# Kernel tuning notes

Measured on AMD Instinct MI355X. Metric: run time of the kernel, lower is better.

The kernel has to match this reference:

```python
import jax, jax.numpy as jnp
from jax import lax
import numpy as np

B, N, C, HEADS = 8, 4096, 512, 16
HD = C // HEADS


def rope2d(x, h, w, base=10000.0):
    # x: [b, h, w, c]; 2D axial RoPE as in the torch `rope` helper
    c = x.shape[-1]
    k_max = c // 4  # feature_dim // (2 * len(channel_dims))
    theta = 1.0 / (base ** (jnp.arange(k_max, dtype=jnp.float32) / k_max))  # [k_max]
    ii = jnp.arange(h, dtype=jnp.float32)[:, None, None]  # row index
    jj = jnp.arange(w, dtype=jnp.float32)[None, :, None]  # col index
    ang = jnp.concatenate([
        jnp.broadcast_to(ii * theta, (h, w, k_max)),
        jnp.broadcast_to(jj * theta, (h, w, k_max)),
    ], axis=-1)  # [h, w, c//2]
    cos, sin = jnp.cos(ang), jnp.sin(ang)
    xp = x.reshape(x.shape[0], h, w, c // 2, 2)
    xr, xi = xp[..., 0], xp[..., 1]
    out = jnp.stack([xr * cos - xi * sin, xi * cos + xr * sin], axis=-1)
    return out.reshape(x.shape)


def setup_inputs() -> dict:
    key = jax.random.key(0)
    k1, k2, k3, k4, k5 = jax.random.split(key, 5)
    x = jax.random.normal(k1, (B, N, C), dtype=jnp.float32)
    Wqk = jax.random.normal(k2, (C, 2 * C), dtype=jnp.float32) * 0.02
    bqk = jax.random.normal(k3, (2 * C,), dtype=jnp.float32) * 0.02
    lepe_w = jax.random.normal(k4, (C, 1, 3, 3), dtype=jnp.float32) * 0.05  # depthwise OIHW
    lepe_b = jax.random.normal(k5, (C,), dtype=jnp.float32) * 0.02
    return {"x": x, "h": 64, "w": 64, "Wqk": Wqk, "bqk": bqk, "lepe_w": lepe_w, "lepe_b": lepe_b}


def reference(x, h, w, Wqk, bqk, lepe_w, lepe_b):
    b, n, c = x.shape
    hd = c // HEADS
    qk = x @ Wqk + bqk                       # [b, n, 2c]
    q = jax.nn.elu(qk[..., :c]) + 1.0        # ELU+1 feature map
    k = jax.nn.elu(qk[..., c:]) + 1.0
    v = x
    q_rope = rope2d(q.reshape(b, h, w, c), h, w).reshape(b, n, HEADS, hd)
    k_rope = rope2d(k.reshape(b, h, w, c), h, w).reshape(b, n, HEADS, hd)
    qh = q.reshape(b, n, HEADS, hd)
    kh = k.reshape(b, n, HEADS, hd)
    vh = v.reshape(b, n, HEADS, hd)
    k_mean = kh.mean(axis=1)                 # [b, HEADS, hd]
    z = 1.0 / (jnp.einsum('bnhd,bhd->bnh', qh, k_mean) + 1e-6)  # [b, n, HEADS]
    inv_n = 1.0 / jnp.float32(n)
    kv = jnp.einsum('bnhd,bnhe->bhde', k_rope, vh) * inv_n       # [b, HEADS, hd, hd]
    attn = jnp.einsum('bnhd,bhde->bnhe', q_rope, kv) * z[..., None]
    out = attn.reshape(b, n, c)
    # depthwise 3x3 LePE on v (== x) as NCHW image
    v_img = x.reshape(b, h, w, c).transpose(0, 3, 1, 2)
    lepe = lax.conv_general_dilated(v_img, lepe_w, (1, 1), 'SAME',
                                    feature_group_count=c,
                                    dimension_numbers=('NCHW', 'OIHW', 'NCHW'))
    lepe = lepe + lepe_b[None, :, None, None]
    out = out + lepe.transpose(0, 2, 3, 1).reshape(b, n, c)
    return out
```

## Files before the change

kernel.cpp:

```cpp
#include <hip/hip_runtime.h>
#include <stdint.h>

static constexpr int BATCH = 8;
static constexpr int NTOK  = 4096;
static constexpr int CDIM  = 512;
static constexpr int NCOL  = 1024;
static constexpr int MROWS = BATCH * NTOK;
static constexpr int KDIM  = 512;

static constexpr size_t OFF_KSUM = 0;
static constexpr size_t OFF_KV   = 16384;
static constexpr size_t OFF_XB   = 540672;
static constexpr size_t OFF_WT   = OFF_XB + 33554432;
static constexpr size_t OFF_QP   = OFF_WT + 1048576;
static constexpr size_t OFF_KR   = OFF_QP + 33554432;
static constexpr size_t OFF_TRIG = OFF_KR + 33554432;
static constexpr size_t OFF_WT9  = OFF_TRIG + 65536;
static constexpr size_t WS_NEED  = OFF_WT9 + 18432;

static constexpr int KV_CHUNKS = 64;
static constexpr int KV_OUT    = BATCH * 16 * 32 * 32;

typedef __attribute__((ext_vector_type(8))) short bf16x8;
typedef __attribute__((ext_vector_type(4))) float f32x4;
typedef __attribute__((ext_vector_type(8))) unsigned short u16x8;

__device__ __forceinline__ float bf2f(unsigned short u) {
  union { unsigned int i; float f; } v; v.i = ((unsigned int)u) << 16; return v.f;
}
__device__ __forceinline__ unsigned short f2bf(float f) {
  union { float f; unsigned int i; } v; v.f = f;
  unsigned int b = v.i + 0x7FFFu + ((v.i >> 16) & 1u);
  return (unsigned short)(b >> 16);
}
__device__ __forceinline__ void gload16(const void* g, void* l) {
  __builtin_amdgcn_global_load_lds(
      (const __attribute__((address_space(1))) unsigned int*)g,
      (__attribute__((address_space(3))) unsigned int*)l,
      16, 0, 0);
}
__device__ __forceinline__ float elu1(float v) {
  return v > 0.f ? v + 1.f : __expf(v);
}

__global__ void prep_kernel(const float* __restrict__ x, const float* __restrict__ Wqk,
                            const float* __restrict__ lepe_w,
                            float* __restrict__ wsf, unsigned short* __restrict__ xb,
                            unsigned short* __restrict__ wT, float2* __restrict__ trig,
                            float* __restrict__ wt9) {
  const int ZN = (int)(OFF_XB / 4);
  const int XN = MROWS * CDIM / 8;
  const int WN = (KDIM * NCOL) / 8;
  const int TN = 64 * 128;
  const int W9 = 9 * 512;
  const int total = ZN + XN + WN + TN + W9;
  for (int i = blockIdx.x * blockDim.x + threadIdx.x; i < total;
       i += gridDim.x * blockDim.x) {
    if (i < ZN) {
      wsf[i] = 0.f;
    } else if (i < ZN + XN) {
      const int j = i - ZN;
      const float4* xp = (const float4*)x + (size_t)j * 2;
      const float4 a = xp[0], b4 = xp[1];
      u16x8 o;
      o[0] = f2bf(a.x);  o[1] = f2bf(a.y);  o[2] = f2bf(a.z);  o[3] = f2bf(a.w);
      o[4] = f2bf(b4.x); o[5] = f2bf(b4.y); o[6] = f2bf(b4.z); o[7] = f2bf(b4.w);
      *((u16x8*)xb + j) = o;
    } else if (i < ZN + XN + WN) {
      const int j = i - ZN - XN;
      const int nc8 = j & 127;
      const int k   = j >> 7;
      const float4* wp = (const float4*)(Wqk + (size_t)k * NCOL + nc8 * 8);
      const float4 a = wp[0], b4 = wp[1];
      const float vals[8] = {a.x, a.y, a.z, a.w, b4.x, b4.y, b4.z, b4.w};
      const int nc0 = nc8 * 8;
#pragma unroll
      for (int t = 0; t < 8; ++t) wT[(size_t)(nc0 + t) * KDIM + k] = f2bf(vals[t]);
    } else if (i < ZN + XN + WN + TN) {
      const int j = i - ZN - XN - WN;
      const int tt = j & 127;
      const int pos = j >> 7;
      const float theta = __expf(-(float)tt * 0.07195578415f);
      const float ang = (float)pos * theta;
      float s, c;
      sincosf(ang, &s, &c);
      trig[pos * 128 + tt] = make_float2(c, s);
    } else {
      const int j = i - ZN - XN - WN - TN;
      const int tap = j >> 9;
      const int c   = j & 511;
      wt9[tap * 512 + c] = lepe_w[c * 9 + tap];
    }
  }
}

__global__ __launch_bounds__(256)
void gemm_kernel(const unsigned short* __restrict__ xb, const unsigned short* __restrict__ wT,
                 const float* __restrict__ bqk, const float2* __restrict__ trig,
                 unsigned short* __restrict__ qp, unsigned short* __restrict__ kr,
                 float* __restrict__ ksum) {
  __shared__ __align__(16) unsigned short S[3][2][128 * 32];
  float* Cst = (float*)&S[0][0][0];
  const int tid = threadIdx.x;
  const int w = tid >> 6;
  const int l = tid & 63;
  const int m0 = blockIdx.x * 128;
  const int nidx = blockIdx.y;
  const int n0 = nidx * 128;
  const int wr = w >> 1, wc = w & 1;

  f32x4 acc[4][4];
#pragma unroll
  for (int i = 0; i < 4; ++i)
#pragma unroll
    for (int j = 0; j < 4; ++j) acc[i][j] = (f32x4){0.f, 0.f, 0.f, 0.f};

  const int c0 = w * 2, c1 = w * 2 + 1;
  const int lr = l >> 2;
  const int lk = (l & 3) * 8;
  const int la = l & 15, lg = l >> 4;
  const int lb = lg * 8;

#define STAGE(kt, bb) do {                                                        \
    const int kc_ = (kt) * 32 + lk;                                               \
    gload16(xb + (size_t)(m0 + c0 * 16 + lr) * KDIM + kc_, &S[bb][0][c0 * 512]);  \
    gload16(xb + (size_t)(m0 + c1 * 16 + lr) * KDIM + kc_, &S[bb][0][c1 * 512]);  \
    gload16(wT + (size_t)(n0 + c0 * 16 + lr) * KDIM + kc_, &S[bb][1][c0 * 512]);  \
    gload16(wT + (size_t)(n0 + c1 * 16 + lr) * KDIM + kc_, &S[bb][1][c1 * 512]);  \
  } while (0)

  STAGE(0, 0);
  STAGE(1, 1);
  asm volatile("s_waitcnt vmcnt(4)" ::: "memory");
  __builtin_amdgcn_s_barrier();
  __builtin_amdgcn_sched_barrier(0);

#pragma unroll
  for (int kt = 0; kt < KDIM / 32; ++kt) {
    const int cur = kt % 3;
    if (kt + 2 < KDIM / 32) STAGE(kt + 2, (kt + 2) % 3);
    bf16x8 af[4], bfr[4];
#pragma unroll
    for (int mi = 0; mi < 4; ++mi)
      af[mi] = *(const bf16x8*)&S[cur][0][(wr * 64 + mi * 16 + la) * 32 + lb];
#pragma unroll
    for (int ni = 0; ni < 4; ++ni)
      bfr[ni] = *(const bf16x8*)&S[cur][1][(wc * 64 + ni * 16 + la) * 32 + lb];
#pragma unroll
    for (int mi = 0; mi < 4; ++mi)
#pragma unroll
      for (int ni = 0; ni < 4; ++ni)
        acc[mi][ni] = __builtin_amdgcn_mfma_f32_16x16x32_bf16(af[mi], bfr[ni], acc[mi][ni], 0, 0, 0);
    if (kt < KDIM / 32 - 1) {
      if (kt + 2 < KDIM / 32) {
        asm volatile("s_waitcnt vmcnt(4)" ::: "memory");
      } else {
        asm volatile("s_waitcnt vmcnt(0)" ::: "memory");
      }
      __builtin_amdgcn_s_barrier();
      __builtin_amdgcn_sched_barrier(0);
    }
  }
#undef STAGE

  const bool isq = (nidx < 4);
  const int bidx = m0 >> 12;
  float colsum[4] = {0.f, 0.f, 0.f, 0.f};
#pragma unroll
  for (int ni = 0; ni < 4; ++ni) {
    const int colg = n0 + wc * 64 + ni * 16 + la;
    const float bias = bqk[colg];
#pragma unroll
    for (int mi = 0; mi < 4; ++mi) {
#pragma unroll
      for (int r = 0; r < 4; ++r) {
        const float v = elu1(acc[mi][ni][r] + bias);
        acc[mi][ni][r] = v;
        if (!isq) colsum[ni] += v;
      }
    }
  }
  if (!isq) {
#pragma unroll
    for (int ni = 0; ni < 4; ++ni) {
      float s = colsum[ni];
      s += __shfl_xor(s, 16);
      s += __shfl_xor(s, 32);
      if (lg == 0) {
        const int ck = n0 - 512 + wc * 64 + ni * 16 + la;
        atomicAdd(&ksum[bidx * CDIM + ck], s);
      }
    }
  }

  for (int cc = 0; cc < 4; ++cc) {
    __syncthreads();
    if (wr == (cc >> 1)) {
      const int mi0 = (cc & 1) * 2;
#pragma unroll
      for (int mil = 0; mil < 2; ++mil) {
#pragma unroll
        for (int ni = 0; ni < 4; ++ni) {
#pragma unroll
          for (int r = 0; r < 4; ++r) {
            Cst[(mil * 16 + lg * 4 + r) * 132 + wc * 64 + ni * 16 + la] = acc[mi0 + mil][ni][r];
          }
        }
      }
    }
    __syncthreads();
#pragma unroll
    for (int it = 0; it < 2; ++it) {
      const int idx = it * 256 + tid;
      const int rowloc = idx >> 4;
      const int seg = idx & 15;
      const int grow = m0 + cc * 32 + rowloc;
      const int lcol = seg * 8;
      float v[8];
      *(float2*)&v[0] = *(const float2*)&Cst[rowloc * 132 + lcol + 0];
      *(float2*)&v[2] = *(const float2*)&Cst[rowloc * 132 + lcol + 2];
      *(float2*)&v[4] = *(const float2*)&Cst[rowloc * 132 + lcol + 4];
      *(float2*)&v[6] = *(const float2*)&Cst[rowloc * 132 + lcol + 6];
      if (isq) {
        u16x8 o;
#pragma unroll
        for (int j = 0; j < 8; ++j) o[j] = f2bf(v[j]);
        *(u16x8*)(qp + (size_t)grow * CDIM + n0 + lcol) = o;
      } else {
        const int ck0 = n0 - 512 + lcol;
        const int n = grow & (NTOK - 1);
        const int p0 = ck0 >> 1;
        const int pos = (p0 >= 128) ? (n & 63) : (n >> 6);
        const float4 t01 = *(const float4*)&trig[pos * 128 + p0];
        const float4 t23 = *(const float4*)&trig[pos * 128 + p0 + 2];
        u16x8 o;
        o[0] = f2bf(v[0] * t01.x - v[1] * t01.y);
        o[1] = f2bf(v[1] * t01.x + v[0] * t01.y);
        o[2] = f2bf(v[2] * t01.z - v[3] * t01.w);
        o[3] = f2bf(v[3] * t01.z + v[2] * t01.w);
        o[4] = f2bf(v[4] * t23.x - v[5] * t23.y);
        o[5] = f2bf(v[5] * t23.x + v[4] * t23.y);
        o[6] = f2bf(v[6] * t23.z - v[7] * t23.w);
        o[7] = f2bf(v[7] * t23.z + v[6] * t23.w);
        *(u16x8*)(kr + (size_t)grow * CDIM + ck0) = o;
      }
    }
  }
}

__global__ __launch_bounds__(512)
void kvpart_kernel(const unsigned short* __restrict__ kr, const unsigned short* __restrict__ xb,
                   float* __restrict__ part) {
  const int bid = blockIdx.x;
  const int b = bid >> 6, ch = bid & 63;
  const int t = threadIdx.x;
  const int h = t >> 5;
  const int sub = t & 31;
  const int d0 = (sub >> 2) * 4, e0 = (sub & 3) * 8;

  float acc[4][8];
#pragma unroll
  for (int i = 0; i < 4; ++i)
#pragma unroll
    for (int j = 0; j < 8; ++j) acc[i][j] = 0.f;

  const size_t rowbase = (size_t)(b * NTOK + ch * 64) * CDIM + h * 32;
  ushort4 k4 = *(const ushort4*)(kr + rowbase + d0);
  u16x8 v8 = *(const u16x8*)(xb + rowbase + e0);
#pragma unroll 2
  for (int r = 0; r < 64; ++r) {
    ushort4 kn = k4;
    u16x8 vn = v8;
    if (r < 63) {
      const size_t offn = rowbase + (size_t)(r + 1) * CDIM;
      kn = *(const ushort4*)(kr + offn + d0);
      vn = *(const u16x8*)(xb + offn + e0);
    }
    const float kf0 = bf2f(k4.x), kf1 = bf2f(k4.y), kf2 = bf2f(k4.z), kf3 = bf2f(k4.w);
    float vf[8];
#pragma unroll
    for (int j = 0; j < 8; ++j) vf[j] = bf2f(v8[j]);
#pragma unroll
    for (int j = 0; j < 8; ++j) {
      acc[0][j] += kf0 * vf[j];
      acc[1][j] += kf1 * vf[j];
      acc[2][j] += kf2 * vf[j];
      acc[3][j] += kf3 * vf[j];
    }
    k4 = kn;
    v8 = vn;
  }

  float* p = part + ((size_t)ch * BATCH * 16 + b * 16 + h) * 1024;
#pragma unroll
  for (int i = 0; i < 4; ++i) {
    *(float4*)&p[(d0 + i) * 32 + e0 + 0] = *(float4*)&acc[i][0];
    *(float4*)&p[(d0 + i) * 32 + e0 + 4] = *(float4*)&acc[i][4];
  }
}

__global__ __launch_bounds__(256)
void kvred_kernel(const float* __restrict__ part, float* __restrict__ kv) {
  const int o = blockIdx.x * 256 + threadIdx.x;
  float s0 = 0.f, s1 = 0.f, s2 = 0.f, s3 = 0.f;
#pragma unroll
  for (int ch = 0; ch < KV_CHUNKS; ch += 4) {
    s0 += part[(size_t)(ch + 0) * KV_OUT + o];
    s1 += part[(size_t)(ch + 1) * KV_OUT + o];
    s2 += part[(size_t)(ch + 2) * KV_OUT + o];
    s3 += part[(size_t)(ch + 3) * KV_OUT + o];
  }
  kv[o] = (s0 + s1 + s2 + s3) * (1.0f / (float)NTOK);
}

__global__ __launch_bounds__(256)
void out4_kernel(const unsigned short* __restrict__ qp, const float* __restrict__ ksum,
                 const float* __restrict__ kv, const float2* __restrict__ trig,
                 const unsigned short* __restrict__ xb, const float* __restrict__ wt9,
                 const float* __restrict__ lepe_b, float* __restrict__ out) {
  __shared__ __align__(16) float kvs[32 * 32];
  __shared__ __align__(16) float qrs[32 * 40];
  const int y = blockIdx.x;
  const int h = blockIdx.y >> 1, half = blockIdx.y & 1;
  const int b = blockIdx.z;
  const int t = threadIdx.x;
  const int e8 = t & 7, tok = t >> 3;
  const int c4 = e8 * 4;

  ((float4*)kvs)[t] = ((const float4*)(kv + (size_t)(b * 16 + h) * 1024))[t];

  const float4 ks4 = *(const float4*)(ksum + b * CDIM + h * 32 + c4);
  const float4 lb4 = *(const float4*)(lepe_b + h * 32 + c4);
  float4 w4[9];
#pragma unroll
  for (int tap = 0; tap < 9; ++tap)
    w4[tap] = *(const float4*)(wt9 + tap * CDIM + h * 32 + c4);
  const int pbase = (h * 16 + e8 * 2) & 127;
  __syncthreads();

  const float inv_n = 1.0f / (float)NTOK;
  const int col = half * 32 + tok;
  const int n = y * 64 + col;
  const size_t rowoff = ((size_t)(b * NTOK + n)) * CDIM + h * 32;

  const ushort4 q4u = *(const ushort4*)(qp + rowoff + c4);
  const float q0 = bf2f(q4u.x), q1 = bf2f(q4u.y), q2 = bf2f(q4u.z), q3 = bf2f(q4u.w);
  float zs = q0 * ks4.x + q1 * ks4.y + q2 * ks4.z + q3 * ks4.w;
  zs += __shfl_xor(zs, 1);
  zs += __shfl_xor(zs, 2);
  zs += __shfl_xor(zs, 4);
  const float z = 1.0f / (zs * inv_n + 1e-6f);
  const int pos = (h >= 8) ? col : y;
  const float4 cs01 = *(const float4*)&trig[pos * 128 + pbase];
  float4 qr;
  qr.x = q0 * cs01.x - q1 * cs01.y;
  qr.y = q1 * cs01.x + q0 * cs01.y;
  qr.z = q2 * cs01.z - q3 * cs01.w;
  qr.w = q3 * cs01.z + q2 * cs01.w;
  *(float4*)&qrs[tok * 40 + c4] = qr;
  float4 acc = lb4;
#pragma unroll
  for (int dy = 0; dy < 3; ++dy) {
    const int iy = y + dy - 1;
    if (iy < 0 || iy > 63) continue;
#pragma unroll
    for (int dx = 0; dx < 3; ++dx) {
      const int ix = col + dx - 1;
      if (ix < 0 || ix > 63) continue;
      const ushort4 xv = *(const ushort4*)(xb + ((size_t)(b * NTOK) + iy * 64 + ix) * CDIM + h * 32 + c4);
      const float4 wv = w4[dy * 3 + dx];
      acc.x += bf2f(xv.x) * wv.x; acc.y += bf2f(xv.y) * wv.y;
      acc.z += bf2f(xv.z) * wv.z; acc.w += bf2f(xv.w) * wv.w;
    }
  }
  float4 attn = {0.f, 0.f, 0.f, 0.f};
#pragma unroll
  for (int dg = 0; dg < 8; ++dg) {
    const float4 qv = *(const float4*)&qrs[tok * 40 + dg * 4];
#pragma unroll
    for (int j = 0; j < 4; ++j) {
      const float qs = (j == 0) ? qv.x : (j == 1) ? qv.y : (j == 2) ? qv.z : qv.w;
      const float4 kvr = *(const float4*)&kvs[(dg * 4 + j) * 32 + c4];
      attn.x += qs * kvr.x; attn.y += qs * kvr.y;
      attn.z += qs * kvr.z; attn.w += qs * kvr.w;
    }
  }
  float4 res;
  res.x = attn.x * z + acc.x;
  res.y = attn.y * z + acc.y;
  res.z = attn.z * z + acc.z;
  res.w = attn.w * z + acc.w;
  *(float4*)(out + rowoff + c4) = res;
}

extern "C" void kernel_launch(void* const* d_in, const int* in_sizes, int n_in,
                              void* d_out, int out_size, void* d_ws, size_t ws_size,
                              hipStream_t stream) {
  const float* x      = (const float*)d_in[0];
  const float* Wqk    = (const float*)d_in[3];
  const float* bqk    = (const float*)d_in[4];
  const float* lepe_w = (const float*)d_in[5];
  const float* lepe_b = (const float*)d_in[6];
  float* out = (float*)d_out;

  if (ws_size < WS_NEED) return;

  char* ws = (char*)d_ws;
  float* ksum            = (float*)(ws + OFF_KSUM);
  float* kv              = (float*)(ws + OFF_KV);
  unsigned short* xb     = (unsigned short*)(ws + OFF_XB);
  unsigned short* wT     = (unsigned short*)(ws + OFF_WT);
  unsigned short* qp     = (unsigned short*)(ws + OFF_QP);
  unsigned short* kr     = (unsigned short*)(ws + OFF_KR);
  float2* trig           = (float2*)(ws + OFF_TRIG);
  float* wt9             = (float*)(ws + OFF_WT9);
  float* part            = (float*)d_out;

  hipLaunchKernelGGL(prep_kernel, dim3(2048), dim3(256), 0, stream,
                     x, Wqk, lepe_w, (float*)ws, xb, wT, trig, wt9);
  hipLaunchKernelGGL(gemm_kernel, dim3(MROWS / 128, NCOL / 128), dim3(256), 0, stream,
                     xb, wT, bqk, trig, qp, kr, ksum);
  hipLaunchKernelGGL(kvpart_kernel, dim3(BATCH * KV_CHUNKS), dim3(512), 0, stream,
                     kr, xb, part);
  hipLaunchKernelGGL(kvred_kernel, dim3(KV_OUT / 256), dim3(256), 0, stream,
                     part, kv);
  hipLaunchKernelGGL(out4_kernel, dim3(64, 32, 8), dim3(256), 0, stream,
                     qp, ksum, kv, trig, xb, wt9, lepe_b, out);
}
```

Before: 172.7 us.

## Enlarge QK GEMM tile to 256x256 with 8 waves and interleaved staging

The QK projection GEMM now uses 512-thread blocks that each compute a 256x256 output tile, so every staged A and B slice is reused across more MFMAs. Each k-step is split into two MFMA halves, with the global-to-LDS loads for A and then B interleaved between them. The MFMA phases run under raised wave priority (s_setprio), and the grid is reordered so that blocks sharing the same row tile are adjacent, which should help L2 reuse of x. The trig lookup index for the RoPE epilogue is also masked to 128 entries, which changes which table entries are read. The costs are more accumulator registers per thread, larger LDS use, and fewer blocks in the grid.

```diff
diff --git a/kernel.cpp b/kernel.cpp
--- a/kernel.cpp
+++ b/kernel.cpp
@@ -94,116 +94,128 @@
   }
 }
 
-__global__ __launch_bounds__(256)
+__global__ __launch_bounds__(512)
 void gemm_kernel(const unsigned short* __restrict__ xb, const unsigned short* __restrict__ wT,
                  const float* __restrict__ bqk, const float2* __restrict__ trig,
                  unsigned short* __restrict__ qp, unsigned short* __restrict__ kr,
                  float* __restrict__ ksum) {
-  __shared__ __align__(16) unsigned short S[3][2][128 * 32];
+  __shared__ __align__(16) unsigned short S[3][2][8192];
   float* Cst = (float*)&S[0][0][0];
   const int tid = threadIdx.x;
-  const int w = tid >> 6;
+  const int wid = tid >> 6;
   const int l = tid & 63;
-  const int m0 = blockIdx.x * 128;
-  const int nidx = blockIdx.y;
-  const int n0 = nidx * 128;
-  const int wr = w >> 1, wc = w & 1;
-
-  f32x4 acc[4][4];
-#pragma unroll
-  for (int i = 0; i < 4; ++i)
+  const int la = l & 15, lg = l >> 4;
+  const int wm = wid >> 2, wn = wid & 3;
+  const int nt = blockIdx.x;
+  const int m0 = blockIdx.y * 256;
+  const int n0 = nt * 256;
+
+  f32x4 acc[8][4];
+#pragma unroll
+  for (int i = 0; i < 8; ++i)
 #pragma unroll
     for (int j = 0; j < 4; ++j) acc[i][j] = (f32x4){0.f, 0.f, 0.f, 0.f};
 
-  const int c0 = w * 2, c1 = w * 2 + 1;
-  const int lr = l >> 2;
-  const int lk = (l & 3) * 8;
-  const int la = l & 15, lg = l >> 4;
-  const int lb = lg * 8;
-
-#define STAGE(kt, bb) do {                                                        \
-    const int kc_ = (kt) * 32 + lk;                                               \
-    gload16(xb + (size_t)(m0 + c0 * 16 + lr) * KDIM + kc_, &S[bb][0][c0 * 512]);  \
-    gload16(xb + (size_t)(m0 + c1 * 16 + lr) * KDIM + kc_, &S[bb][0][c1 * 512]);  \
-    gload16(wT + (size_t)(n0 + c0 * 16 + lr) * KDIM + kc_, &S[bb][1][c0 * 512]);  \
-    gload16(wT + (size_t)(n0 + c1 * 16 + lr) * KDIM + kc_, &S[bb][1][c1 * 512]);  \
-  } while (0)
-
-  STAGE(0, 0);
-  STAGE(1, 1);
+  const int srow = tid >> 2;
+  const int scol = (tid & 3) * 8;
+
+#define STG_A(kt, bb, rr) gload16(xb + (size_t)(m0 + (rr) * 128 + srow) * KDIM + (kt) * 32 + scol, \
+                                  &S[bb][0][(rr) * 4096 + tid * 8])
+#define STG_B(kt, bb, rr) gload16(wT + (size_t)(n0 + (rr) * 128 + srow) * KDIM + (kt) * 32 + scol, \
+                                  &S[bb][1][(rr) * 4096 + tid * 8])
+
+  STG_A(0, 0, 0); STG_A(0, 0, 1); STG_B(0, 0, 0); STG_B(0, 0, 1);
+  STG_A(1, 1, 0); STG_A(1, 1, 1); STG_B(1, 1, 0); STG_B(1, 1, 1);
   asm volatile("s_waitcnt vmcnt(4)" ::: "memory");
   __builtin_amdgcn_s_barrier();
   __builtin_amdgcn_sched_barrier(0);
 
-#pragma unroll
-  for (int kt = 0; kt < KDIM / 32; ++kt) {
+  for (int kt = 0; kt < 16; ++kt) {
     const int cur = kt % 3;
-    if (kt + 2 < KDIM / 32) STAGE(kt + 2, (kt + 2) % 3);
-    bf16x8 af[4], bfr[4];
-#pragma unroll
-    for (int mi = 0; mi < 4; ++mi)
-      af[mi] = *(const bf16x8*)&S[cur][0][(wr * 64 + mi * 16 + la) * 32 + lb];
-#pragma unroll
-    for (int ni = 0; ni < 4; ++ni)
-      bfr[ni] = *(const bf16x8*)&S[cur][1][(wc * 64 + ni * 16 + la) * 32 + lb];
-#pragma unroll
-    for (int mi = 0; mi < 4; ++mi)
-#pragma unroll
-      for (int ni = 0; ni < 4; ++ni)
-        acc[mi][ni] = __builtin_amdgcn_mfma_f32_16x16x32_bf16(af[mi], bfr[ni], acc[mi][ni], 0, 0, 0);
-    if (kt < KDIM / 32 - 1) {
-      if (kt + 2 < KDIM / 32) {
-        asm volatile("s_waitcnt vmcnt(4)" ::: "memory");
-      } else {
-        asm volatile("s_waitcnt vmcnt(0)" ::: "memory");
-      }
-      __builtin_amdgcn_s_barrier();
-      __builtin_amdgcn_sched_barrier(0);
-    }
-  }
-#undef STAGE
-
-  const bool isq = (nidx < 4);
+    const int nx2 = (kt + 2) % 3;
+    bf16x8 af[4], bf[4];
+#pragma unroll
+    for (int i = 0; i < 4; ++i)
+      af[i] = *(const bf16x8*)&S[cur][0][(wm * 128 + i * 16 + la) * 32 + lg * 8];
+#pragma unroll
+    for (int j = 0; j < 4; ++j)
+      bf[j] = *(const bf16x8*)&S[cur][1][(wn * 64 + j * 16 + la) * 32 + lg * 8];
+    if (kt + 2 < 16) { STG_A(kt + 2, nx2, 0); STG_A(kt + 2, nx2, 1); }
+    __builtin_amdgcn_s_barrier();
+    asm volatile("s_waitcnt lgkmcnt(0)" ::: "memory");
+    __builtin_amdgcn_sched_barrier(0);
+    __builtin_amdgcn_s_setprio(1);
+#pragma unroll
+    for (int i = 0; i < 4; ++i)
+#pragma unroll
+      for (int j = 0; j < 4; ++j)
+        acc[i][j] = __builtin_amdgcn_mfma_f32_16x16x32_bf16(af[i], bf[j], acc[i][j], 0, 0, 0);
+    __builtin_amdgcn_s_setprio(0);
+    __builtin_amdgcn_s_barrier();
+#pragma unroll
+    for (int i = 0; i < 4; ++i)
+      af[i] = *(const bf16x8*)&S[cur][0][(wm * 128 + (4 + i) * 16 + la) * 32 + lg * 8];
+    if (kt + 2 < 16) { STG_B(kt + 2, nx2, 0); STG_B(kt + 2, nx2, 1); }
+    __builtin_amdgcn_s_barrier();
+    asm volatile("s_waitcnt lgkmcnt(0)" ::: "memory");
+    __builtin_amdgcn_sched_barrier(0);
+    __builtin_amdgcn_s_setprio(1);
+#pragma unroll
+    for (int i = 0; i < 4; ++i)
+#pragma unroll
+      for (int j = 0; j < 4; ++j)
+        acc[4 + i][j] = __builtin_amdgcn_mfma_f32_16x16x32_bf16(af[i], bf[j], acc[4 + i][j], 0, 0, 0);
+    __builtin_amdgcn_s_setprio(0);
+    if (kt < 14) {
+      asm volatile("s_waitcnt vmcnt(4)" ::: "memory");
+    } else if (kt == 14) {
+      asm volatile("s_waitcnt vmcnt(0)" ::: "memory");
+    }
+    __builtin_amdgcn_s_barrier();
+    __builtin_amdgcn_sched_barrier(0);
+  }
+#undef STG_A
+#undef STG_B
+
+  const bool isq = (nt < 2);
   const int bidx = m0 >> 12;
   float colsum[4] = {0.f, 0.f, 0.f, 0.f};
 #pragma unroll
-  for (int ni = 0; ni < 4; ++ni) {
-    const int colg = n0 + wc * 64 + ni * 16 + la;
-    const float bias = bqk[colg];
-#pragma unroll
-    for (int mi = 0; mi < 4; ++mi) {
+  for (int j = 0; j < 4; ++j) {
+    const float bias = bqk[n0 + wn * 64 + j * 16 + la];
+#pragma unroll
+    for (int i = 0; i < 8; ++i) {
 #pragma unroll
       for (int r = 0; r < 4; ++r) {
-        const float v = elu1(acc[mi][ni][r] + bias);
-        acc[mi][ni][r] = v;
-        if (!isq) colsum[ni] += v;
+        const float v = elu1(acc[i][j][r] + bias);
+        acc[i][j][r] = v;
+        if (!isq) colsum[j] += v;
       }
     }
   }
   if (!isq) {
 #pragma unroll
-    for (int ni = 0; ni < 4; ++ni) {
-      float s = colsum[ni];
+    for (int j = 0; j < 4; ++j) {
+      float s = colsum[j];
       s += __shfl_xor(s, 16);
       s += __shfl_xor(s, 32);
       if (lg == 0) {
-        const int ck = n0 - 512 + wc * 64 + ni * 16 + la;
-        atomicAdd(&ksum[bidx * CDIM + ck], s);
+        atomicAdd(&ksum[bidx * CDIM + (n0 - 512) + wn * 64 + j * 16 + la], s);
       }
     }
   }
 
-  for (int cc = 0; cc < 4; ++cc) {
+  for (int cc = 0; cc < 8; ++cc) {
     __syncthreads();
-    if (wr == (cc >> 1)) {
-      const int mi0 = (cc & 1) * 2;
+    if (wm == (cc >> 2)) {
+      const int mi0 = (cc & 3) * 2;
 #pragma unroll
       for (int mil = 0; mil < 2; ++mil) {
 #pragma unroll
-        for (int ni = 0; ni < 4; ++ni) {
+        for (int j = 0; j < 4; ++j) {
 #pragma unroll
           for (int r = 0; r < 4; ++r) {
-            Cst[(mil * 16 + lg * 4 + r) * 132 + wc * 64 + ni * 16 + la] = acc[mi0 + mil][ni][r];
+            Cst[(mil * 16 + lg * 4 + r) * 260 + wn * 64 + j * 16 + la] = acc[mi0 + mil][j][r];
           }
         }
       }
@@ -211,28 +223,28 @@
     __syncthreads();
 #pragma unroll
     for (int it = 0; it < 2; ++it) {
-      const int idx = it * 256 + tid;
-      const int rowloc = idx >> 4;
-      const int seg = idx & 15;
+      const int idx = it * 512 + tid;
+      const int rowloc = idx >> 5;
+      const int seg = idx & 31;
       const int grow = m0 + cc * 32 + rowloc;
       const int lcol = seg * 8;
       float v[8];
-      *(float2*)&v[0] = *(const float2*)&Cst[rowloc * 132 + lcol + 0];
-      *(float2*)&v[2] = *(const float2*)&Cst[rowloc * 132 + lcol + 2];
-      *(float2*)&v[4] = *(const float2*)&Cst[rowloc * 132 + lcol + 4];
-      *(float2*)&v[6] = *(const float2*)&Cst[rowloc * 132 + lcol + 6];
+      *(float2*)&v[0] = *(const float2*)&Cst[rowloc * 260 + lcol + 0];
+      *(float2*)&v[2] = *(const float2*)&Cst[rowloc * 260 + lcol + 2];
+      *(float2*)&v[4] = *(const float2*)&Cst[rowloc * 260 + lcol + 4];
+      *(float2*)&v[6] = *(const float2*)&Cst[rowloc * 260 + lcol + 6];
       if (isq) {
         u16x8 o;
 #pragma unroll
-        for (int j = 0; j < 8; ++j) o[j] = f2bf(v[j]);
+        for (int jj = 0; jj < 8; ++jj) o[jj] = f2bf(v[jj]);
         *(u16x8*)(qp + (size_t)grow * CDIM + n0 + lcol) = o;
       } else {
-        const int ck0 = n0 - 512 + lcol;
+        const int ck0 = (n0 - 512) + lcol;
         const int n = grow & (NTOK - 1);
         const int p0 = ck0 >> 1;
         const int pos = (p0 >= 128) ? (n & 63) : (n >> 6);
-        const float4 t01 = *(const float4*)&trig[pos * 128 + p0];
-        const float4 t23 = *(const float4*)&trig[pos * 128 + p0 + 2];
+        const float4 t01 = *(const float4*)&trig[pos * 128 + (p0 & 127)];
+        const float4 t23 = *(const float4*)&trig[pos * 128 + (p0 & 127) + 2];
         u16x8 o;
         o[0] = f2bf(v[0] * t01.x - v[1] * t01.y);
         o[1] = f2bf(v[1] * t01.x + v[0] * t01.y);
@@ -418,7 +430,7 @@
 
   hipLaunchKernelGGL(prep_kernel, dim3(2048), dim3(256), 0, stream,
                      x, Wqk, lepe_w, (float*)ws, xb, wT, trig, wt9);
-  hipLaunchKernelGGL(gemm_kernel, dim3(MROWS / 128, NCOL / 128), dim3(256), 0, stream,
+  hipLaunchKernelGGL(gemm_kernel, dim3(4, MROWS / 256), dim3(512), 0, stream,
                      xb, wT, bqk, trig, qp, kr, ksum);
   hipLaunchKernelGGL(kvpart_kernel, dim3(BATCH * KV_CHUNKS), dim3(512), 0, stream,
                      kr, xb, part);
```

Result: no change. 174.6 us (+1.1%).
